# Kernel optimization log

Measured on AMD Instinct MI355X. Metric: run time of the kernel, lower is better.

Reference implementation:

```python
import jax, jax.numpy as jnp
import numpy as np

B, T, N, C_IN, H, CHEB_K, E_DIM = 64, 64, 512, 1, 32, 2, 10


def setup_inputs() -> dict:
    key = jax.random.key(0)
    k1, k2, k3, k4 = jax.random.split(key, 4)
    return {
        "x": jax.random.normal(k1, (B, T, N, C_IN), dtype=jnp.float32),
        "init_state": jnp.zeros((1, B, 2, N, H), dtype=jnp.float32),
        "node_embeddings": jax.random.normal(k2, (N, E_DIM), dtype=jnp.float32),
        "mask": jnp.ones((N, N), dtype=jnp.float32),
        "weights_pool": jax.random.normal(k3, (E_DIM, CHEB_K, C_IN + H, 4 * H), dtype=jnp.float32) * 0.1,
        "bias_pool": jax.random.normal(k4, (E_DIM, 4 * H), dtype=jnp.float32) * 0.1,
    }


def reference(x, init_state, node_embeddings, mask, weights_pool, bias_pool):
    n = node_embeddings.shape[0]
    cheb_k = weights_pool.shape[1]
    # Adaptive adjacency (AGCRN-style), masked.
    A = jax.nn.softmax(jax.nn.relu(node_embeddings @ node_embeddings.T), axis=1) * mask
    # Chebyshev support set: T0 = I, T1 = A, Tk = 2 A T_{k-1} - T_{k-2}
    supports = [jnp.eye(n, dtype=A.dtype), A]
    for _ in range(2, cheb_k):
        supports.append(2.0 * (A @ supports[-1]) - supports[-2])
    supports = jnp.stack(supports[:cheb_k])  # [K, N, N]
    # Node-adaptive gate weights/bias.
    weights = jnp.einsum('nd,dkio->nkio', node_embeddings, weights_pool)  # [N,K,Cin+H,4H]
    bias = node_embeddings @ bias_pool  # [N, 4H]
    hdim = bias.shape[-1] // 4

    h0 = init_state[0, :, 0]  # [B, N, H]
    c0 = init_state[0, :, 1]  # [B, N, H]

    def step(carry, x_t):
        h, c = carry
        z = jnp.concatenate([x_t, h], axis=-1)              # [B, N, Cin+H]
        zg = jnp.einsum('knm,bmc->bnkc', supports, z)        # graph conv over cheb orders
        gates = jnp.einsum('bnkc,nkco->bno', zg, weights) + bias  # [B, N, 4H]
        i, f, o, g = jnp.split(gates, 4, axis=-1)
        c_new = jax.nn.sigmoid(f) * c + jax.nn.sigmoid(i) * jnp.tanh(g)
        h_new = jax.nn.sigmoid(o) * jnp.tanh(c_new)
        return (h_new, c_new), h_new

    (_, _), hs = jax.lax.scan(step, (h0, c0), jnp.moveaxis(x, 1, 0))
    return jnp.moveaxis(hs, 0, 1)  # [B, T, N, H]
```

## Files before the change

### kernel.cpp

```cpp
#include <hip/hip_runtime.h>
#include <math.h>

#define BB 64
#define TT 64
#define NN 512
#define HH 32
#define CC 33
#define EE 10
#define GG 128
#define AZS2 (NN * 2048)
#define KS 4


__global__ __launch_bounds__(256) void k_A(const float* __restrict__ E,
                                           const float* __restrict__ mask,
                                           float* __restrict__ A) {
  __shared__ float sE[NN * EE];
  __shared__ float red[256];
  int tid = threadIdx.x, n = blockIdx.x;
  for (int i = tid; i < NN * EE; i += 256) sE[i] = E[i];
  __syncthreads();
  float en[EE];
#pragma unroll
  for (int d = 0; d < EE; ++d) en[d] = sE[n * EE + d];
  float sv[2];
  float mx = -1e30f;
#pragma unroll
  for (int r = 0; r < 2; ++r) {
    int m = tid + r * 256;
    float s = 0.f;
#pragma unroll
    for (int d = 0; d < EE; ++d) s += en[d] * sE[m * EE + d];
    s = fmaxf(s, 0.f);
    sv[r] = s;
    mx = fmaxf(mx, s);
  }
  red[tid] = mx; __syncthreads();
  for (int s = 128; s > 0; s >>= 1) {
    if (tid < s) red[tid] = fmaxf(red[tid], red[tid + s]);
    __syncthreads();
  }
  mx = red[0]; __syncthreads();
  float sum = 0.f;
#pragma unroll
  for (int r = 0; r < 2; ++r) { sv[r] = expf(sv[r] - mx); sum += sv[r]; }
  red[tid] = sum; __syncthreads();
  for (int s = 128; s > 0; s >>= 1) {
    if (tid < s) red[tid] += red[tid + s];
    __syncthreads();
  }
  float inv = 1.f / red[0];
#pragma unroll
  for (int r = 0; r < 2; ++r) {
    int m = tid + r * 256;
    A[n * NN + m] = sv[r] * inv * mask[n * NN + m];
  }
}

__global__ __launch_bounds__(256) void k_Wb(const float* __restrict__ E,
                                            const float* __restrict__ Wp,
                                            const float* __restrict__ bp,
                                            float* __restrict__ Wp2,
                                            float* __restrict__ bias) {
  int tid = threadIdx.x, n = blockIdx.x;
  float e[EE];
#pragma unroll
  for (int d = 0; d < EE; ++d) e[d] = E[n * EE + d];
  for (int i = tid; i < 2 * CC * GG; i += 256) {
    float acc = 0.f;
#pragma unroll
    for (int d = 0; d < EE; ++d) acc += e[d] * Wp[d * (2 * CC * GG) + i];
    int r = i >> 7, o = i & 127, g = o >> 5, hh = o & 31;
    Wp2[(size_t)n * 8448 + r * 128 + hh * 4 + g] = acc;
  }
  if (tid < GG) {
    float acc = 0.f;
#pragma unroll
    for (int d = 0; d < EE; ++d) acc += e[d] * bp[d * GG + tid];
    bias[n * GG + tid] = acc;
  }
}

__global__ __launch_bounds__(256) void k_xt(const float* __restrict__ x,
                                            float* __restrict__ xt) {
  __shared__ float tile[64][65];
  int tid = threadIdx.x;
  int t = blockIdx.x >> 3, m0 = (blockIdx.x & 7) << 6;
  int l16 = tid & 15, grp = tid >> 4;
#pragma unroll
  for (int r = 0; r < 4; ++r) {
    int b = r * 16 + grp;
    float4 v = *reinterpret_cast<const float4*>(&x[(b * TT + t) * NN + m0 + l16 * 4]);
    tile[b][l16 * 4 + 0] = v.x; tile[b][l16 * 4 + 1] = v.y;
    tile[b][l16 * 4 + 2] = v.z; tile[b][l16 * 4 + 3] = v.w;
  }
  __syncthreads();
#pragma unroll
  for (int r = 0; r < 4; ++r) {
    int m = r * 16 + grp;
    float4 v;
    v.x = tile[l16 * 4 + 0][m]; v.y = tile[l16 * 4 + 1][m];
    v.z = tile[l16 * 4 + 2][m]; v.w = tile[l16 * 4 + 3][m];
    *reinterpret_cast<float4*>(&xt[(t * NN + m0 + m) * BB + l16 * 4]) = v;
  }
}

__global__ __launch_bounds__(256) void k_ax(const float* __restrict__ A,
                                            const float* __restrict__ xt,
                                            float* __restrict__ ax) {
  __shared__ float As[32][68];
  __shared__ float Bs[32][64];
  int tid = threadIdx.x;
  int t = blockIdx.x;
  int n0 = blockIdx.y * 64;
  int tx = tid & 15, ty = tid >> 4;
  int arow = tid >> 2, akc = (tid & 3) * 4;
  int bcol4 = tid & 15, brow0 = tid >> 4;
  float acc[4][4] = {};
  for (int k0 = 0; k0 < NN; k0 += 32) {
    float4 a0 = *reinterpret_cast<const float4*>(&A[(n0 + arow) * NN + k0 + akc]);
    float4 a1 = *reinterpret_cast<const float4*>(&A[(n0 + arow) * NN + k0 + 16 + akc]);
    As[akc + 0][arow] = a0.x; As[akc + 1][arow] = a0.y;
    As[akc + 2][arow] = a0.z; As[akc + 3][arow] = a0.w;
    As[16 + akc + 0][arow] = a1.x; As[16 + akc + 1][arow] = a1.y;
    As[16 + akc + 2][arow] = a1.z; As[16 + akc + 3][arow] = a1.w;
#pragma unroll
    for (int p = 0; p < 2; ++p) {
      int brow = brow0 + p * 16;
      float4 b4 = *reinterpret_cast<const float4*>(&xt[(t * NN + k0 + brow) * BB + bcol4 * 4]);
      *reinterpret_cast<float4*>(&Bs[brow][bcol4 * 4]) = b4;
    }
    __syncthreads();
#pragma unroll
    for (int kk = 0; kk < 32; ++kk) {
      float4 av = *reinterpret_cast<const float4*>(&As[kk][ty * 4]);
      float4 bv = *reinterpret_cast<const float4*>(&Bs[kk][tx * 4]);
      float a[4] = {av.x, av.y, av.z, av.w};
      float b[4] = {bv.x, bv.y, bv.z, bv.w};
#pragma unroll
      for (int i = 0; i < 4; ++i)
#pragma unroll
        for (int j = 0; j < 4; ++j) acc[i][j] += a[i] * b[j];
    }
    __syncthreads();
  }
#pragma unroll
  for (int i = 0; i < 4; ++i) {
    float4 v = {acc[i][0], acc[i][1], acc[i][2], acc[i][3]};
    *reinterpret_cast<float4*>(&ax[(size_t)(t * NN + n0 + ty * 4 + i) * BB + tx * 4]) = v;
  }
}

__global__ __launch_bounds__(256) void k_init(const float* __restrict__ init,
                                              float* __restrict__ h,
                                              float* __restrict__ c) {
  int i = blockIdx.x * 256 + threadIdx.x;
  if (i >= NN * BB * HH) return;
  int n = i >> 11, r = i & 2047, b = r >> 5, hh = r & 31;
  h[i] = init[((b * 2 + 0) * NN + n) * HH + hh];
  c[i] = init[((b * 2 + 1) * NN + n) * HH + hh];
}

__global__ __launch_bounds__(512, 1) void k_gemmP(
    const float* __restrict__ A, const float* __restrict__ h,
    float* __restrict__ az2) {
  __shared__ float Asp[128 * 132];
  __shared__ float Bs[32 * 132];
  const int tid = threadIdx.x;
  const int j0 = blockIdx.x * 128;
  const int n0 = blockIdx.y * 128;
  const int kz = blockIdx.z;
  const int kbase = kz * 128;
  const int tx = tid & 31, ty = tid >> 5;
  const int skr = tid >> 4, scg = tid & 15;

  {
    int row = tid >> 2, q4 = tid & 3;
#pragma unroll
    for (int p = 0; p < 8; ++p) {
      int kk = q4 * 32 + p * 4;
      float4 a = *reinterpret_cast<const float4*>(
          &A[(size_t)(n0 + row) * NN + kbase + kk]);
      Asp[(kk + 0) * 132 + row] = a.x;
      Asp[(kk + 1) * 132 + row] = a.y;
      Asp[(kk + 2) * 132 + row] = a.z;
      Asp[(kk + 3) * 132 + row] = a.w;
    }
  }
  __syncthreads();

  float acc[8][4];
#pragma unroll
  for (int i = 0; i < 8; ++i)
#pragma unroll
    for (int j = 0; j < 4; ++j) acc[i][j] = 0.f;
#pragma unroll 1
  for (int kt = 0; kt < 4; ++kt) {
    {
      const float* hsrc = &h[(size_t)(kbase + kt * 32 + skr) * 2048 + j0 + scg * 8];
      float4 v0 = *reinterpret_cast<const float4*>(hsrc);
      float4 v1 = *reinterpret_cast<const float4*>(hsrc + 4);
      float* bd = &Bs[skr * 132 + scg * 8];
      *reinterpret_cast<float4*>(bd) = v0;
      *reinterpret_cast<float4*>(bd + 4) = v1;
    }
    __syncthreads();
#pragma unroll 4
    for (int kk = 0; kk < 32; ++kk) {
      int k = kt * 32 + kk;
      float4 a0 = *reinterpret_cast<const float4*>(&Asp[k * 132 + ty * 8]);
      float4 a1 = *reinterpret_cast<const float4*>(&Asp[k * 132 + ty * 8 + 4]);
      float4 b4 = *reinterpret_cast<const float4*>(&Bs[kk * 132 + tx * 4]);
      float av[8] = {a0.x, a0.y, a0.z, a0.w, a1.x, a1.y, a1.z, a1.w};
      float bv[4] = {b4.x, b4.y, b4.z, b4.w};
#pragma unroll
      for (int i = 0; i < 8; ++i)
#pragma unroll
        for (int j = 0; j < 4; ++j) acc[i][j] += av[i] * bv[j];
    }
    __syncthreads();
  }
  {
    float* dst = az2 + (size_t)kz * AZS2 + (size_t)(n0 + ty * 8) * 2048 + j0 + tx * 4;
#pragma unroll
    for (int i = 0; i < 8; ++i) {
      float4 v = {acc[i][0], acc[i][1], acc[i][2], acc[i][3]};
      *reinterpret_cast<float4*>(dst + (size_t)i * 2048) = v;
    }
  }
}

__global__ __launch_bounds__(256) void k_stepP(
    const float* __restrict__ xt, const float* __restrict__ ax,
    const float* __restrict__ Wp2, const float* __restrict__ bias,
    const float* __restrict__ az2, float* __restrict__ h,
    float* __restrict__ c, float* __restrict__ out, int t) {
  __shared__ float zl[66 * 68];
  const int tid = threadIdx.x, n = blockIdx.x;
  const int bhh = tid & 31, boct = tid >> 5;

  for (int i = tid; i < BB * HH; i += 256) {
    int b = i >> 5, hh = i & 31;
    zl[(1 + hh) * 68 + b] = h[(size_t)n * 2048 + i];
    float s = az2[(size_t)n * 2048 + i];
#pragma unroll
    for (int kz = 1; kz < KS; ++kz)
      s += az2[(size_t)kz * AZS2 + (size_t)n * 2048 + i];
    zl[(34 + hh) * 68 + b] = s;
  }
  if (tid < BB) {
    zl[0 * 68 + tid]  = xt[(size_t)(t * NN + n) * BB + tid];
    zl[33 * 68 + tid] = ax[(size_t)(t * NN + n) * BB + tid];
  }
  __syncthreads();

  float accB[8][4];
#pragma unroll
  for (int g = 0; g < 4; ++g) {
    float bv = bias[n * GG + g * 32 + bhh];
#pragma unroll
    for (int b8 = 0; b8 < 8; ++b8) accB[b8][g] = bv;
  }
  const float* wb = Wp2 + (size_t)n * 8448 + bhh * 4;
  const float* zb2 = &zl[boct * 8];
#pragma unroll 2
  for (int r = 0; r < 66; ++r) {
    float4 w4 = *reinterpret_cast<const float4*>(&wb[r * 128]);
    float4 za = *reinterpret_cast<const float4*>(&zb2[r * 68]);
    float4 zb = *reinterpret_cast<const float4*>(&zb2[r * 68 + 4]);
    float zv[8] = {za.x, za.y, za.z, za.w, zb.x, zb.y, zb.z, zb.w};
#pragma unroll
    for (int b8 = 0; b8 < 8; ++b8) {
      accB[b8][0] += zv[b8] * w4.x;
      accB[b8][1] += zv[b8] * w4.y;
      accB[b8][2] += zv[b8] * w4.z;
      accB[b8][3] += zv[b8] * w4.w;
    }
  }
#pragma unroll
  for (int b8 = 0; b8 < 8; ++b8) {
    int bg = boct * 8 + b8;
    int io = n * 2048 + bg * 32 + bhh;
    float cold = c[io];
    float si = 1.f / (1.f + expf(-accB[b8][0]));
    float sf = 1.f / (1.f + expf(-accB[b8][1]));
    float so = 1.f / (1.f + expf(-accB[b8][2]));
    float cn = sf * cold + si * tanhf(accB[b8][3]);
    float hn = so * tanhf(cn);
    c[io] = cn;
    h[io] = hn;
    out[((size_t)(bg * TT + t) * NN + n) * HH + bhh] = hn;
  }
}

extern "C" void kernel_launch(void* const* d_in, const int* in_sizes, int n_in,
                              void* d_out, int out_size, void* d_ws, size_t ws_size,
                              hipStream_t stream) {
  const float* x    = (const float*)d_in[0];
  const float* init = (const float*)d_in[1];
  const float* E    = (const float*)d_in[2];
  const float* mask = (const float*)d_in[3];
  const float* Wp   = (const float*)d_in[4];
  const float* bp   = (const float*)d_in[5];
  float* out = (float*)d_out;
  float* ws = (float*)d_ws;
  float* A    = ws;
  float* Wp2  = A + NN * NN;
  float* bias = Wp2 + NN * 2 * CC * GG;
  float* xt   = bias + NN * GG;
  float* ax   = xt + TT * NN * BB;
  float* h    = ax + TT * NN * BB;
  float* c    = h + NN * BB * HH;
  float* az2  = c + NN * BB * HH;

  k_A<<<NN, 256, 0, stream>>>(E, mask, A);
  k_Wb<<<NN, 256, 0, stream>>>(E, Wp, bp, Wp2, bias);
  k_xt<<<TT * 8, 256, 0, stream>>>(x, xt);
  k_ax<<<dim3(TT, 8), 256, 0, stream>>>(A, xt, ax);
  k_init<<<(NN * BB * HH + 255) / 256, 256, 0, stream>>>(init, h, c);

  for (int t = 0; t < TT; ++t) {
    k_gemmP<<<dim3(16, 4, KS), 512, 0, stream>>>(A, h, az2);
    k_stepP<<<NN, 256, 0, stream>>>(xt, ax, Wp2, bias, az2, h, c, out, t);
  }
}
```

Before: 2.814 ms.

## Run per-step A·h GEMM on bf16 MFMA with three-way split emulating fp32

The per-timestep graph-conv GEMM (A times hidden state) moves from scalar FP32 FMA to bf16 MFMA matrix instructions. Both operands are split into three bf16 pieces (hi, mid, lo) and six cross-product MFMAs keep accuracy close to fp32. A's split is computed once in k_A. h is split on the fly while staging into LDS, transposed into a k-contiguous layout. This trades extra conversion work, LDS traffic and MFMA count for much higher matrix-core throughput on the dominant recurrent GEMM.

```diff
diff --git a/kernel.cpp b/kernel.cpp
--- a/kernel.cpp
+++ b/kernel.cpp
@@ -10,11 +10,27 @@
 #define GG 128
 #define AZS2 (NN * 2048)
 #define KS 4
+#define BP 72
+
+typedef __attribute__((ext_vector_type(8))) short short8;
+typedef __attribute__((ext_vector_type(4))) float f32x4;
+
+__device__ __forceinline__ unsigned short f2b(float f) {
+  unsigned int x = __float_as_uint(f);
+  x += 0x7fff + ((x >> 16) & 1);
+  return (unsigned short)(x >> 16);
+}
+__device__ __forceinline__ float b2f(unsigned short u) {
+  return __uint_as_float(((unsigned int)u) << 16);
+}
 
 
 __global__ __launch_bounds__(256) void k_A(const float* __restrict__ E,
                                            const float* __restrict__ mask,
-                                           float* __restrict__ A) {
+                                           float* __restrict__ A,
+                                           unsigned short* __restrict__ A1,
+                                           unsigned short* __restrict__ A2,
+                                           unsigned short* __restrict__ A3) {
   __shared__ float sE[NN * EE];
   __shared__ float red[256];
   int tid = threadIdx.x, n = blockIdx.x;
@@ -53,7 +69,15 @@
 #pragma unroll
   for (int r = 0; r < 2; ++r) {
     int m = tid + r * 256;
-    A[n * NN + m] = sv[r] * inv * mask[n * NN + m];
+    float a = sv[r] * inv * mask[n * NN + m];
+    A[n * NN + m] = a;
+    unsigned short u1 = f2b(a);
+    float r1 = a - b2f(u1);
+    unsigned short u2 = f2b(r1);
+    float r2 = r1 - b2f(u2);
+    A1[n * NN + m] = u1;
+    A2[n * NN + m] = u2;
+    A3[n * NN + m] = f2b(r2);
   }
 }
 
@@ -161,73 +185,107 @@
   c[i] = init[((b * 2 + 1) * NN + n) * HH + hh];
 }
 
-__global__ __launch_bounds__(512, 1) void k_gemmP(
-    const float* __restrict__ A, const float* __restrict__ h,
+__global__ __launch_bounds__(512, 1) void k_gemmM(
+    const unsigned short* __restrict__ A1, const unsigned short* __restrict__ A2,
+    const unsigned short* __restrict__ A3, const float* __restrict__ h,
     float* __restrict__ az2) {
-  __shared__ float Asp[128 * 132];
-  __shared__ float Bs[32 * 132];
+  __shared__ unsigned short lds[6 * 128 * BP];
+  unsigned short* As1 = lds;
+  unsigned short* As2 = As1 + 128 * BP;
+  unsigned short* As3 = As2 + 128 * BP;
+  unsigned short* Bs1 = As3 + 128 * BP;
+  unsigned short* Bs2 = Bs1 + 128 * BP;
+  unsigned short* Bs3 = Bs2 + 128 * BP;
   const int tid = threadIdx.x;
   const int j0 = blockIdx.x * 128;
   const int n0 = blockIdx.y * 128;
   const int kz = blockIdx.z;
-  const int kbase = kz * 128;
-  const int tx = tid & 31, ty = tid >> 5;
-  const int skr = tid >> 4, scg = tid & 15;
-
-  {
-    int row = tid >> 2, q4 = tid & 3;
-#pragma unroll
-    for (int p = 0; p < 8; ++p) {
-      int kk = q4 * 32 + p * 4;
-      float4 a = *reinterpret_cast<const float4*>(
-          &A[(size_t)(n0 + row) * NN + kbase + kk]);
-      Asp[(kk + 0) * 132 + row] = a.x;
-      Asp[(kk + 1) * 132 + row] = a.y;
-      Asp[(kk + 2) * 132 + row] = a.z;
-      Asp[(kk + 3) * 132 + row] = a.w;
-    }
-  }
-  __syncthreads();
-
-  float acc[8][4];
-#pragma unroll
-  for (int i = 0; i < 8; ++i)
-#pragma unroll
-    for (int j = 0; j < 4; ++j) acc[i][j] = 0.f;
+  const int arow = tid >> 2, aseg = tid & 3;
+  const int bkp = tid >> 4, bjq = tid & 15;
+  const int w = tid >> 6, l = tid & 63;
+  const int rowbase = (w & 3) * 32, colbase = (w >> 2) * 64;
+  const int fr = l & 15, fg = l >> 4;
+
+  f32x4 acc[2][4];
+#pragma unroll
+  for (int rt = 0; rt < 2; ++rt)
+#pragma unroll
+    for (int ct = 0; ct < 4; ++ct) acc[rt][ct] = (f32x4){0.f, 0.f, 0.f, 0.f};
+
 #pragma unroll 1
-  for (int kt = 0; kt < 4; ++kt) {
+  for (int half = 0; half < 2; ++half) {
+    const int kb2 = kz * 128 + half * 64;
     {
-      const float* hsrc = &h[(size_t)(kbase + kt * 32 + skr) * 2048 + j0 + scg * 8];
-      float4 v0 = *reinterpret_cast<const float4*>(hsrc);
-      float4 v1 = *reinterpret_cast<const float4*>(hsrc + 4);
-      float* bd = &Bs[skr * 132 + scg * 8];
-      *reinterpret_cast<float4*>(bd) = v0;
-      *reinterpret_cast<float4*>(bd + 4) = v1;
-    }
-    __syncthreads();
-#pragma unroll 4
-    for (int kk = 0; kk < 32; ++kk) {
-      int k = kt * 32 + kk;
-      float4 a0 = *reinterpret_cast<const float4*>(&Asp[k * 132 + ty * 8]);
-      float4 a1 = *reinterpret_cast<const float4*>(&Asp[k * 132 + ty * 8 + 4]);
-      float4 b4 = *reinterpret_cast<const float4*>(&Bs[kk * 132 + tx * 4]);
-      float av[8] = {a0.x, a0.y, a0.z, a0.w, a1.x, a1.y, a1.z, a1.w};
-      float bv[4] = {b4.x, b4.y, b4.z, b4.w};
-#pragma unroll
-      for (int i = 0; i < 8; ++i)
-#pragma unroll
-        for (int j = 0; j < 4; ++j) acc[i][j] += av[i] * bv[j];
-    }
-    __syncthreads();
-  }
-  {
-    float* dst = az2 + (size_t)kz * AZS2 + (size_t)(n0 + ty * 8) * 2048 + j0 + tx * 4;
-#pragma unroll
-    for (int i = 0; i < 8; ++i) {
-      float4 v = {acc[i][0], acc[i][1], acc[i][2], acc[i][3]};
-      *reinterpret_cast<float4*>(dst + (size_t)i * 2048) = v;
-    }
-  }
+      const size_t gb = (size_t)(n0 + arow) * NN + kb2 + aseg * 16;
+      unsigned short* d1 = &As1[arow * BP + aseg * 16];
+      unsigned short* d2 = &As2[arow * BP + aseg * 16];
+      unsigned short* d3 = &As3[arow * BP + aseg * 16];
+#pragma unroll
+      for (int p = 0; p < 2; ++p) {
+        *reinterpret_cast<short8*>(d1 + p * 8) = *reinterpret_cast<const short8*>(&A1[gb + p * 8]);
+        *reinterpret_cast<short8*>(d2 + p * 8) = *reinterpret_cast<const short8*>(&A2[gb + p * 8]);
+        *reinterpret_cast<short8*>(d3 + p * 8) = *reinterpret_cast<const short8*>(&A3[gb + p * 8]);
+      }
+    }
+    {
+      const float* h0 = &h[(size_t)(kb2 + 2 * bkp) * 2048 + j0 + bjq];
+      const float* h1 = h0 + 2048;
+#pragma unroll
+      for (int q = 0; q < 8; ++q) {
+        float v0 = h0[q * 16], v1 = h1[q * 16];
+        unsigned short p01 = f2b(v0), p11 = f2b(v1);
+        float s0 = v0 - b2f(p01), s1 = v1 - b2f(p11);
+        unsigned short p02 = f2b(s0), p12 = f2b(s1);
+        unsigned short p03 = f2b(s0 - b2f(p02)), p13 = f2b(s1 - b2f(p12));
+        int off = (bjq + 16 * q) * BP + 2 * bkp;
+        *reinterpret_cast<unsigned int*>(&Bs1[off]) = (unsigned int)p01 | ((unsigned int)p11 << 16);
+        *reinterpret_cast<unsigned int*>(&Bs2[off]) = (unsigned int)p02 | ((unsigned int)p12 << 16);
+        *reinterpret_cast<unsigned int*>(&Bs3[off]) = (unsigned int)p03 | ((unsigned int)p13 << 16);
+      }
+    }
+    __syncthreads();
+#pragma unroll
+    for (int ks = 0; ks < 2; ++ks) {
+      short8 a1f[2], a2f[2], a3f[2], b1f[4], b2f4[4], b3f[4];
+#pragma unroll
+      for (int rt = 0; rt < 2; ++rt) {
+        int off = (rowbase + rt * 16 + fr) * BP + ks * 32 + fg * 8;
+        a1f[rt] = *reinterpret_cast<const short8*>(&As1[off]);
+        a2f[rt] = *reinterpret_cast<const short8*>(&As2[off]);
+        a3f[rt] = *reinterpret_cast<const short8*>(&As3[off]);
+      }
+#pragma unroll
+      for (int ct = 0; ct < 4; ++ct) {
+        int off = (colbase + ct * 16 + fr) * BP + ks * 32 + fg * 8;
+        b1f[ct] = *reinterpret_cast<const short8*>(&Bs1[off]);
+        b2f4[ct] = *reinterpret_cast<const short8*>(&Bs2[off]);
+        b3f[ct] = *reinterpret_cast<const short8*>(&Bs3[off]);
+      }
+#pragma unroll
+      for (int rt = 0; rt < 2; ++rt)
+#pragma unroll
+        for (int ct = 0; ct < 4; ++ct) {
+          f32x4 a = acc[rt][ct];
+          a = __builtin_amdgcn_mfma_f32_16x16x32_bf16(a1f[rt], b1f[ct], a, 0, 0, 0);
+          a = __builtin_amdgcn_mfma_f32_16x16x32_bf16(a1f[rt], b2f4[ct], a, 0, 0, 0);
+          a = __builtin_amdgcn_mfma_f32_16x16x32_bf16(a2f[rt], b1f[ct], a, 0, 0, 0);
+          a = __builtin_amdgcn_mfma_f32_16x16x32_bf16(a1f[rt], b3f[ct], a, 0, 0, 0);
+          a = __builtin_amdgcn_mfma_f32_16x16x32_bf16(a2f[rt], b2f4[ct], a, 0, 0, 0);
+          a = __builtin_amdgcn_mfma_f32_16x16x32_bf16(a3f[rt], b1f[ct], a, 0, 0, 0);
+          acc[rt][ct] = a;
+        }
+    }
+    __syncthreads();
+  }
+  float* dst = az2 + (size_t)kz * AZS2;
+#pragma unroll
+  for (int rt = 0; rt < 2; ++rt)
+#pragma unroll
+    for (int ct = 0; ct < 4; ++ct)
+#pragma unroll
+      for (int r = 0; r < 4; ++r)
+        dst[(size_t)(n0 + rowbase + rt * 16 + fg * 4 + r) * 2048 +
+            j0 + colbase + ct * 16 + fr] = acc[rt][ct][r];
 }
 
 __global__ __launch_bounds__(256) void k_stepP(
@@ -305,7 +363,10 @@
   float* out = (float*)d_out;
   float* ws = (float*)d_ws;
   float* A    = ws;
-  float* Wp2  = A + NN * NN;
+  unsigned short* A1 = (unsigned short*)(A + NN * NN);
+  unsigned short* A2 = A1 + NN * NN;
+  unsigned short* A3 = A2 + NN * NN;
+  float* Wp2  = (float*)(A3 + NN * NN);
   float* bias = Wp2 + NN * 2 * CC * GG;
   float* xt   = bias + NN * GG;
   float* ax   = xt + TT * NN * BB;
@@ -313,14 +374,14 @@
   float* c    = h + NN * BB * HH;
   float* az2  = c + NN * BB * HH;
 
-  k_A<<<NN, 256, 0, stream>>>(E, mask, A);
+  k_A<<<NN, 256, 0, stream>>>(E, mask, A, A1, A2, A3);
   k_Wb<<<NN, 256, 0, stream>>>(E, Wp, bp, Wp2, bias);
   k_xt<<<TT * 8, 256, 0, stream>>>(x, xt);
   k_ax<<<dim3(TT, 8), 256, 0, stream>>>(A, xt, ax);
   k_init<<<(NN * BB * HH + 255) / 256, 256, 0, stream>>>(init, h, c);
 
   for (int t = 0; t < TT; ++t) {
-    k_gemmP<<<dim3(16, 4, KS), 512, 0, stream>>>(A, h, az2);
+    k_gemmM<<<dim3(16, 4, KS), 512, 0, stream>>>(A1, A2, A3, h, az2);
     k_stepP<<<NN, 256, 0, stream>>>(xt, ax, Wp2, bias, az2, h, c, out, t);
   }
 }
```

New measurement: 2.312 ms. 17.8% less time.
